# Kernel tuning notes

Measured on AMD Instinct MI355X. Metric: run time of the kernel, lower is better.

The kernel has to match this reference:

```python
import jax, jax.numpy as jnp
import numpy as np
from jax import lax

BIN_NUM = 48
CPG = BIN_NUM * 3            # 144 hidden channels
NOUT = BIN_NUM + 1           # 49 symbols
K = 5                        # masked conv kernel size
H, W = 256, 512
TABLE_TOTAL = 65536.0        # EntropyTable total frequency
SCALE = 2.0 / (BIN_NUM - 1.0)


def _causal_mask(include_center: bool) -> jnp.ndarray:
    # Raster-scan causal 5x5 mask: all rows above center, left of center in
    # center row; center tap only for 'hidden' (mask-B) layers.
    m = np.zeros((K, K), np.float32)
    c = K // 2
    m[:c, :] = 1.0
    m[c, :c] = 1.0
    if include_center:
        m[c, c] = 1.0
    return jnp.asarray(m)[None, None]  # broadcast over (O, I, kh, kw)


def _mconv(x, w, b, mask):
    # x: (N, C, H, W); w: (O, I, K, K)
    y = lax.conv_general_dilated(
        x, w * mask, window_strides=(1, 1), padding='SAME',
        dimension_numbers=('NCHW', 'OIHW', 'NCHW'))
    return y + b[None, :, None, None]


def setup_inputs() -> dict:
    key = jax.random.key(0)
    ks = jax.random.split(key, 8)
    # quantized code indices in [0, BIN_NUM)
    data = jax.random.randint(ks[0], (1, 1, H, W), 0, BIN_NUM).astype(jnp.float32)
    s0 = 1.0 / np.sqrt(1 * K * K)
    sr = 1.0 / np.sqrt(CPG * K * K)
    w0 = jax.random.normal(ks[1], (CPG, 1, K, K), jnp.float32) * s0
    b0 = jnp.zeros((CPG,), jnp.float32)
    # 5 residual blocks x 2 convs = 10 hidden masked convs, stacked
    wres = jax.random.normal(ks[2], (10, CPG, CPG, K, K), jnp.float32) * sr
    bres = jnp.zeros((10, CPG), jnp.float32)
    wl = jax.random.normal(ks[3], (NOUT, CPG, K, K), jnp.float32) * sr
    bl = jnp.zeros((NOUT,), jnp.float32)
    return {"data": data, "w0": w0, "b0": b0, "wres": wres, "bres": bres,
            "wl": wl, "bl": bl}


def reference(data, w0, b0, wres, bres, wl, bl):
    mask_a = _causal_mask(False)   # first layer excludes center pixel
    mask_b = _causal_mask(True)    # hidden layers include center pixel

    # Scale(-1, 2/(bin_num-1)): map codes [0, bin_num-1] -> [-1, 1]
    x = data * SCALE - 1.0
    x = jax.nn.relu(_mconv(x, w0, b0, mask_a))
    # 5 residual blocks: y = relu(conv(relu(conv(x)))) + x
    for i in range(5):
        h1 = jax.nn.relu(_mconv(x, wres[2 * i], bres[2 * i], mask_b))
        h2 = jax.nn.relu(_mconv(h1, wres[2 * i + 1], bres[2 * i + 1], mask_b))
        x = x + h2
    logits = _mconv(x, wl, bl, mask_b)          # (1, 49, H, W)

    # EntropyTable: per-pixel softmax -> cumulative frequency table (total 65536)
    probs = jax.nn.softmax(logits, axis=1)
    cdf = jnp.cumsum(probs, axis=1) * TABLE_TOTAL
    zeros = jnp.zeros((cdf.shape[0], 1) + cdf.shape[2:], cdf.dtype)
    vec = jnp.concatenate([zeros, cdf], axis=1)  # (1, 50, H, W)
    return vec
```

## Files before the change

### kernel.cpp

```cpp
#include <hip/hip_runtime.h>

#define HH 256
#define WW 512
#define CPG 144
#define NKG 18
#define WP 516
#define HPADR 258
#define XB_E ((size_t)NKG * HPADR * WP * 8)
#define NCH 59
#define KREAL 1872
#define SCALE_F (2.0f / 47.0f)

typedef __attribute__((ext_vector_type(8))) short short8;
typedef __attribute__((ext_vector_type(4))) float floatx4;

__device__ __forceinline__ unsigned short f2bf(float f) {
    unsigned u = __builtin_bit_cast(unsigned, f);
    u += 0x7FFFu + ((u >> 16) & 1u);
    return (unsigned short)(u >> 16);
}
__device__ __forceinline__ float bf2f(unsigned short h) {
    unsigned u = ((unsigned)h) << 16;
    return __builtin_bit_cast(float, u);
}
__device__ __forceinline__ void async16(const void* g, void* l) {
    __builtin_amdgcn_global_load_lds(
        (const __attribute__((address_space(1))) unsigned int*)g,
        (__attribute__((address_space(3))) unsigned int*)l, 16, 0, 0);
}
__device__ __forceinline__ void tap_decode(int t, int& kh, int& kw) {
    kh = t < 5 ? 0 : (t < 10 ? 1 : 2);
    kw = t - (t < 5 ? 0 : (t < 10 ? 5 : 10));
}
__device__ __forceinline__ unsigned aoff(int c, int lg) {
    int g = c * 4 + lg;
    if (g > 233) g = 233;
    int t = (g * 57) >> 10;
    int kgp = g - t * 18;
    int kh, kw; tap_decode(t, kh, kw);
    return (unsigned)(((kgp * 4 + kh) * 132 + kw) * 16);
}

__global__ void k_zero(float* __restrict__ p, size_t n4) {
    size_t i = (size_t)blockIdx.x * blockDim.x + threadIdx.x;
    size_t stride = (size_t)gridDim.x * blockDim.x;
    float4 z = make_float4(0.f, 0.f, 0.f, 0.f);
    for (; i < n4; i += stride) ((float4*)p)[i] = z;
}

__global__ void k_pack_hidden(const float* __restrict__ wres, unsigned short* __restrict__ wpk) {
    const int total = 10 * NCH * CPG * 32;
    int i = blockIdx.x * blockDim.x + threadIdx.x;
    int stride = gridDim.x * blockDim.x;
    for (; i < total; i += stride) {
        int kk = i & 31;
        int q  = i >> 5;
        int co = q % CPG;
        int c  = (q / CPG) % NCH;
        int l  = q / (CPG * NCH);
        int K = c * 32 + kk;
        float v = 0.f;
        if (K < KREAL) {
            int t = K / CPG, ci = K - t * CPG;
            int kh, kw; tap_decode(t, kh, kw);
            v = wres[(((size_t)(l * CPG + co) * CPG + ci) * 5 + kh) * 5 + kw];
        }
        wpk[i] = f2bf(v);
    }
}
__global__ void k_pack_final(const float* __restrict__ wl, unsigned short* __restrict__ wpkF) {
    const int total = NCH * 64 * 32;
    int i = blockIdx.x * blockDim.x + threadIdx.x;
    if (i >= total) return;
    int kk = i & 31;
    int co = (i >> 5) & 63;
    int c  = i >> 11;
    int K = c * 32 + kk;
    float v = 0.f;
    if (K < KREAL && co < 49) {
        int t = K / CPG, ci = K - t * CPG;
        int kh, kw; tap_decode(t, kh, kw);
        v = wl[(((size_t)co * CPG + ci) * 5 + kh) * 5 + kw];
    }
    wpkF[i] = f2bf(v);
}
__global__ void k_pack_small(const float* __restrict__ w0, const float* __restrict__ bl,
                             float* __restrict__ w0p, float* __restrict__ blp) {
    int i = blockIdx.x * blockDim.x + threadIdx.x;
    if (i < 12 * CPG) {
        int co = i % CPG, t = i / CPG;
        int kh, kw; tap_decode(t, kh, kw);
        w0p[i] = w0[co * 25 + kh * 5 + kw];
    } else if (i < 12 * CPG + 64) {
        int k = i - 12 * CPG;
        blp[k] = k < 49 ? bl[k] : 0.f;
    }
}

__global__ __launch_bounds__(384) void k_layer0(
    const float* __restrict__ data, const float* __restrict__ w0p,
    const float* __restrict__ b0, unsigned short* __restrict__ Xb) {
    const int lane = threadIdx.x;
    const int x = blockIdx.x * 64 + lane;
    const int y = blockIdx.y;

    float xv[12];
#pragma unroll
    for (int t = 0; t < 12; t++) {
        int kh, kw; tap_decode(t, kh, kw);
        int yy = y + kh - 2, xx = x + kw - 2;
        xv[t] = (yy >= 0 && xx >= 0 && xx < WW) ? data[yy * WW + xx] * SCALE_F - 1.0f : 0.f;
    }
#pragma unroll
    for (int kgi = 0; kgi < 3; kgi++) {
        int kg = threadIdx.y * 3 + kgi;
        float a8[8];
#pragma unroll
        for (int j = 0; j < 8; j++) a8[j] = 0.f;
#pragma unroll
        for (int t = 0; t < 12; t++)
#pragma unroll
            for (int j = 0; j < 8; j++)
                a8[j] = fmaf(w0p[t * CPG + kg * 8 + j], xv[t], a8[j]);
        short8 o;
#pragma unroll
        for (int j = 0; j < 8; j++)
            o[j] = (short)f2bf(fmaxf(a8[j] + b0[kg * 8 + j], 0.f));
        *(short8*)&Xb[((size_t)(kg * HPADR + y + 2) * WP + (x + 2)) * 8] = o;
    }
}

template<bool RES>
__global__ __launch_bounds__(768, 3) void k_conv(
    const unsigned short* __restrict__ in,
    const unsigned short* __restrict__ wq,
    const float* __restrict__ bias,
    const unsigned short* __restrict__ res,
    unsigned short* __restrict__ out) {
    __shared__ __align__(16) unsigned short As[NKG][4][132][8];
    const int tid  = threadIdx.x;
    const int lane = tid & 63;
    const int wid  = tid >> 6;
    const int ng   = wid % 3;
    const int r    = (wid / 3) & 1;
    const int ph   = wid / 6;
    const int lr = lane & 15;
    const int lg = lane >> 4;

    const int fid = blockIdx.x + (int)gridDim.x * blockIdx.y;
    const int swz = (fid & 7) * 64 + (fid >> 3);
    const int x0 = (swz & 3) * 128;
    const int y0 = (swz >> 2) * 2;

    floatx4 acc[4][3];
#pragma unroll
    for (int m = 0; m < 4; m++)
#pragma unroll
        for (int n = 0; n < 3; n++) acc[m][n] = (floatx4)0.f;

    for (int i = wid; i < 144; i += 12) {
        int half = i & 1;
        int rr   = (i >> 1) & 3;
        int kg   = i >> 3;
        async16(in + ((size_t)(kg * HPADR + y0 + rr) * WP + x0 + half * 64 + lane) * 8,
                &As[kg][rr][half * 64][0]);
    }
    if (tid < 288) {
        int kg = tid >> 4;
        int rr = (tid >> 2) & 3;
        int pxl = 128 + (tid & 3);
        *(short8*)&As[kg][rr][pxl][0] =
            *(const short8*)(in + ((size_t)(kg * HPADR + y0 + rr) * WP + x0 + pxl) * 8);
    }
    asm volatile("s_waitcnt vmcnt(0) lgkmcnt(0)" ::: "memory");
    __builtin_amdgcn_s_barrier();
    __builtin_amdgcn_sched_barrier(0);

    const char* abase = (const char*)&As[0][r][ph * 64 + lr][0];
    auto LDA = [&](int c, short8 (&a)[4]) {
        const char* ap = abase + aoff(c, lg);
#pragma unroll
        for (int m = 0; m < 4; ++m) a[m] = *(const short8*)(ap + m * 256);
    };
    auto LDB = [&](int c, short8 (&b)[3]) {
        const unsigned short* bp = wq + (size_t)c * 4608 + (ng * 48 + lr) * 32 + lg * 8;
#pragma unroll
        for (int n = 0; n < 3; ++n) b[n] = *(const short8*)(bp + n * 512);
    };
    auto CMP = [&](const short8 (&a)[4], const short8 (&b)[3]) {
        __builtin_amdgcn_sched_barrier(0);
        __builtin_amdgcn_s_setprio(1);
#pragma unroll
        for (int m = 0; m < 4; ++m)
#pragma unroll
            for (int n = 0; n < 3; ++n)
                acc[m][n] = __builtin_amdgcn_mfma_f32_16x16x32_bf16(a[m], b[n], acc[m][n], 0, 0, 0);
        __builtin_amdgcn_s_setprio(0);
        __builtin_amdgcn_sched_barrier(0);
    };

    short8 A0[4], A1[4], B0[3], B1[3], B2[3], B3[3];
    LDB(0, B0); LDB(1, B1); LDA(0, A0);
#pragma unroll 1
    for (int c = 0; c < 56; c += 4) {
        LDB(c + 2, B2); LDB(c + 3, B3);
        LDA(c + 1, A1); CMP(A0, B0);
        LDA(c + 2, A0); CMP(A1, B1);
        LDB(c + 4, B0); LDB(c + 5, B1);
        LDA(c + 3, A1); CMP(A0, B2);
        LDA(c + 4, A0); CMP(A1, B3);
    }
    LDB(58, B2);
    LDA(57, A1); CMP(A0, B0);
    LDA(58, A0); CMP(A1, B1);
    CMP(A0, B2);

#pragma unroll
    for (int n = 0; n < 3; ++n) {
        int co = ng * 48 + n * 16 + lr;
        float bv = bias[co];
        const size_t pb = ((size_t)((co >> 3) * HPADR + y0 + 2 + r) * WP + (x0 + 2)) * 8 + (co & 7);
#pragma unroll
        for (int m = 0; m < 4; ++m)
#pragma unroll
            for (int rr = 0; rr < 4; ++rr) {
                int px = ph * 64 + m * 16 + lg * 4 + rr;
                size_t o = pb + (size_t)px * 8;
                float v = fmaxf(acc[m][n][rr] + bv, 0.f);
                if (RES) v += bf2f(res[o]);
                out[o] = f2bf(v);
            }
    }
}

__global__ __launch_bounds__(512, 2) void k_logits(
    const unsigned short* __restrict__ in,
    const unsigned short* __restrict__ wq,
    const float* __restrict__ blp,
    float* __restrict__ logits) {
    __shared__ __align__(16) unsigned short As[NKG][4][132][8];
    const int tid  = threadIdx.x;
    const int lane = tid & 63;
    const int wid  = tid >> 6;
    const int ng   = wid & 1;
    const int r    = (wid >> 1) & 1;
    const int ph   = wid >> 2;
    const int lr = lane & 15;
    const int lg = lane >> 4;

    const int fid = blockIdx.x + (int)gridDim.x * blockIdx.y;
    const int swz = (fid & 7) * 64 + (fid >> 3);
    const int x0 = (swz & 3) * 128;
    const int y0 = (swz >> 2) * 2;

    floatx4 acc[4][2];
#pragma unroll
    for (int m = 0; m < 4; m++)
#pragma unroll
        for (int n = 0; n < 2; n++) acc[m][n] = (floatx4)0.f;

    for (int i = wid; i < 144; i += 8) {
        int half = i & 1;
        int rr   = (i >> 1) & 3;
        int kg   = i >> 3;
        async16(in + ((size_t)(kg * HPADR + y0 + rr) * WP + x0 + half * 64 + lane) * 8,
                &As[kg][rr][half * 64][0]);
    }
    if (tid < 288) {
        int kg = tid >> 4;
        int rr = (tid >> 2) & 3;
        int pxl = 128 + (tid & 3);
        *(short8*)&As[kg][rr][pxl][0] =
            *(const short8*)(in + ((size_t)(kg * HPADR + y0 + rr) * WP + x0 + pxl) * 8);
    }
    asm volatile("s_waitcnt vmcnt(0) lgkmcnt(0)" ::: "memory");
    __builtin_amdgcn_s_barrier();
    __builtin_amdgcn_sched_barrier(0);

    const char* abase = (const char*)&As[0][r][ph * 64 + lr][0];
    auto LDA = [&](int c, short8 (&a)[4]) {
        const char* ap = abase + aoff(c, lg);
#pragma unroll
        for (int m = 0; m < 4; ++m) a[m] = *(const short8*)(ap + m * 256);
    };
    auto LDB = [&](int c, short8 (&b)[2]) {
        const unsigned short* bp = wq + (size_t)c * 2048 + (ng * 32 + lr) * 32 + lg * 8;
#pragma unroll
        for (int n = 0; n < 2; ++n) b[n] = *(const short8*)(bp + n * 512);
    };
    auto CMP = [&](const short8 (&a)[4], const short8 (&b)[2]) {
        __builtin_amdgcn_sched_barrier(0);
        __builtin_amdgcn_s_setprio(1);
#pragma unroll
        for (int m = 0; m < 4; ++m)
#pragma unroll
            for (int n = 0; n < 2; ++n)
                acc[m][n] = __builtin_amdgcn_mfma_f32_16x16x32_bf16(a[m], b[n], acc[m][n], 0, 0, 0);
        __builtin_amdgcn_s_setprio(0);
        __builtin_amdgcn_sched_barrier(0);
    };

    short8 A0[4], A1[4], B0[2], B1[2], B2[2], B3[2];
    LDB(0, B0); LDB(1, B1); LDA(0, A0);
#pragma unroll 1
    for (int c = 0; c < 56; c += 4) {
        LDB(c + 2, B2); LDB(c + 3, B3);
        LDA(c + 1, A1); CMP(A0, B0);
        LDA(c + 2, A0); CMP(A1, B1);
        LDB(c + 4, B0); LDB(c + 5, B1);
        LDA(c + 3, A1); CMP(A0, B2);
        LDA(c + 4, A0); CMP(A1, B3);
    }
    LDB(58, B2);
    LDA(57, A1); CMP(A0, B0);
    LDA(58, A0); CMP(A1, B1);
    CMP(A0, B2);

#pragma unroll
    for (int n = 0; n < 2; ++n) {
        int co = ng * 32 + n * 16 + lr;
        float bv = blp[co];
#pragma unroll
        for (int m = 0; m < 4; ++m)
#pragma unroll
            for (int rr = 0; rr < 4; ++rr) {
                int px = ph * 64 + m * 16 + lg * 4 + rr;
                logits[((size_t)(y0 + r) * WW + x0 + px) * 64 + co] = acc[m][n][rr] + bv;
            }
    }
}

__global__ __launch_bounds__(256) void k_softmax(
    const float* __restrict__ lg, float* __restrict__ out) {
    const int px = blockIdx.x * 256 + threadIdx.x;
    const int y = blockIdx.y;
    const size_t p = (size_t)y * WW + px;
    const float* l = lg + p * 64;
    float v[49];
    float m = -1e30f;
#pragma unroll
    for (int k = 0; k < 49; k++) { v[k] = l[k]; m = fmaxf(m, v[k]); }
    float s = 0.f;
#pragma unroll
    for (int k = 0; k < 49; k++) {
        v[k] = exp2f((v[k] - m) * 1.44269504088896f);
        s += v[k];
    }
    const float inv = 65536.0f / s;
    out[p] = 0.f;
    float run = 0.f;
#pragma unroll
    for (int k = 0; k < 49; k++) {
        run += v[k];
        out[(size_t)(k + 1) * (HH * WW) + p] = run * inv;
    }
}

extern "C" void kernel_launch(void* const* d_in, const int* in_sizes, int n_in,
                              void* d_out, int out_size, void* d_ws, size_t ws_size,
                              hipStream_t stream) {
    (void)in_sizes; (void)n_in; (void)out_size; (void)ws_size;
    const float* data = (const float*)d_in[0];
    const float* w0   = (const float*)d_in[1];
    const float* b0   = (const float*)d_in[2];
    const float* wres = (const float*)d_in[3];
    const float* bres = (const float*)d_in[4];
    const float* wl   = (const float*)d_in[5];
    const float* bl   = (const float*)d_in[6];
    float* out = (float*)d_out;

    char* ws = (char*)d_ws;
    unsigned short* Xb   = (unsigned short*)ws;
    unsigned short* Hb   = Xb + XB_E;
    unsigned short* wpk  = Hb + XB_E;
    unsigned short* wpkF = wpk + (size_t)10 * NCH * CPG * 32;
    float* blp  = (float*)(wpkF + (size_t)NCH * 64 * 32);
    float* w0p  = blp + 64;
    float* logits = w0p + 1728;

    k_zero<<<2048, 256, 0, stream>>>((float*)ws, (2 * XB_E * 2) / 16);

    k_pack_hidden<<<2048, 256, 0, stream>>>(wres, wpk);
    k_pack_final<<<(NCH * 64 * 32 + 255) / 256, 256, 0, stream>>>(wl, wpkF);
    k_pack_small<<<7, 256, 0, stream>>>(w0, bl, w0p, blp);

    k_layer0<<<dim3(8, 256), dim3(64, 6), 0, stream>>>(data, w0p, b0, Xb);

    const size_t LSTRIDE = (size_t)NCH * CPG * 32;
    for (int i = 0; i < 5; i++) {
        k_conv<false><<<dim3(4, 128), 768, 0, stream>>>(
            Xb, wpk + (size_t)(2 * i) * LSTRIDE, bres + (2 * i) * CPG, Xb, Hb);
        k_conv<true><<<dim3(4, 128), 768, 0, stream>>>(
            Hb, wpk + (size_t)(2 * i + 1) * LSTRIDE, bres + (2 * i + 1) * CPG, Xb, Xb);
    }

    k_logits<<<dim3(4, 128), 512, 0, stream>>>(Xb, wpkF, blp, logits);
    k_softmax<<<dim3(2, 256), 256, 0, stream>>>(logits, out);
}
```

Before: 913.5 us.

## Retile convs to 4x64 pixel blocks and stage weights in LDS with triple buffering

```diff
diff --git a/kernel.cpp b/kernel.cpp
--- a/kernel.cpp
+++ b/kernel.cpp
@@ -32,13 +32,13 @@
     kh = t < 5 ? 0 : (t < 10 ? 1 : 2);
     kw = t - (t < 5 ? 0 : (t < 10 ? 5 : 10));
 }
-__device__ __forceinline__ unsigned aoff(int c, int lg) {
+__device__ __forceinline__ unsigned aoff6(int c, int lg) {
     int g = c * 4 + lg;
     if (g > 233) g = 233;
     int t = (g * 57) >> 10;
     int kgp = g - t * 18;
     int kh, kw; tap_decode(t, kh, kw);
-    return (unsigned)(((kgp * 4 + kh) * 132 + kw) * 16);
+    return (unsigned)(((kgp * 6 + kh) * 68 + kw) * 16);
 }
 
 __global__ void k_zero(float* __restrict__ p, size_t n4) {
@@ -49,16 +49,17 @@
 }
 
 __global__ void k_pack_hidden(const float* __restrict__ wres, unsigned short* __restrict__ wpk) {
-    const int total = 10 * NCH * CPG * 32;
+    const int total = 10 * NCH * 4 * CPG * 8;
     int i = blockIdx.x * blockDim.x + threadIdx.x;
     int stride = gridDim.x * blockDim.x;
     for (; i < total; i += stride) {
-        int kk = i & 31;
-        int q  = i >> 5;
-        int co = q % CPG;
-        int c  = (q / CPG) % NCH;
-        int l  = q / (CPG * NCH);
-        int K = c * 32 + kk;
+        int j  = i & 7;
+        int q  = i >> 3;
+        int co = q % CPG;  q /= CPG;
+        int lg = q & 3;    q >>= 2;
+        int c  = q % NCH;
+        int l  = q / NCH;
+        int K = c * 32 + lg * 8 + j;
         float v = 0.f;
         if (K < KREAL) {
             int t = K / CPG, ci = K - t * CPG;
@@ -69,13 +70,14 @@
     }
 }
 __global__ void k_pack_final(const float* __restrict__ wl, unsigned short* __restrict__ wpkF) {
-    const int total = NCH * 64 * 32;
+    const int total = NCH * 4 * 64 * 8;
     int i = blockIdx.x * blockDim.x + threadIdx.x;
     if (i >= total) return;
-    int kk = i & 31;
-    int co = (i >> 5) & 63;
+    int j  = i & 7;
+    int co = (i >> 3) & 63;
+    int lg = (i >> 9) & 3;
     int c  = i >> 11;
-    int K = c * 32 + kk;
+    int K = c * 32 + lg * 8 + j;
     float v = 0.f;
     if (K < KREAL && co < 49) {
         int t = K / CPG, ci = K - t * CPG;
@@ -137,20 +139,20 @@
     const float* __restrict__ bias,
     const unsigned short* __restrict__ res,
     unsigned short* __restrict__ out) {
-    __shared__ __align__(16) unsigned short As[NKG][4][132][8];
+    __shared__ __align__(16) unsigned short As[NKG][6][68][8];
+    __shared__ __align__(16) unsigned short Bs[3][4608];
     const int tid  = threadIdx.x;
     const int lane = tid & 63;
     const int wid  = tid >> 6;
     const int ng   = wid % 3;
-    const int r    = (wid / 3) & 1;
-    const int ph   = wid / 6;
+    const int r    = wid / 3;
     const int lr = lane & 15;
     const int lg = lane >> 4;
 
     const int fid = blockIdx.x + (int)gridDim.x * blockIdx.y;
     const int swz = (fid & 7) * 64 + (fid >> 3);
-    const int x0 = (swz & 3) * 128;
-    const int y0 = (swz >> 2) * 2;
+    const int x0 = (swz & 7) * 64;
+    const int y0 = (swz >> 3) * 4;
 
     floatx4 acc[4][3];
 #pragma unroll
@@ -158,37 +160,41 @@
 #pragma unroll
         for (int n = 0; n < 3; n++) acc[m][n] = (floatx4)0.f;
 
-    for (int i = wid; i < 144; i += 12) {
-        int half = i & 1;
-        int rr   = (i >> 1) & 3;
-        int kg   = i >> 3;
-        async16(in + ((size_t)(kg * HPADR + y0 + rr) * WP + x0 + half * 64 + lane) * 8,
-                &As[kg][rr][half * 64][0]);
-    }
-    if (tid < 288) {
-        int kg = tid >> 4;
-        int rr = (tid >> 2) & 3;
-        int pxl = 128 + (tid & 3);
-        *(short8*)&As[kg][rr][pxl][0] =
-            *(const short8*)(in + ((size_t)(kg * HPADR + y0 + rr) * WP + x0 + pxl) * 8);
+    for (int i = wid; i < 108; i += 12) {
+        int kg = i / 6, rr = i - (i / 6) * 6;
+        async16(in + ((size_t)(kg * HPADR + y0 + rr) * WP + x0 + lane) * 8,
+                &As[kg][rr][0][0]);
+    }
+    if (tid < 432) {
+        int kg = tid / 24;
+        int rem = tid - kg * 24;
+        int rr = rem >> 2;
+        int p  = rem & 3;
+        *(short8*)&As[kg][rr][64 + p][0] =
+            *(const short8*)(in + ((size_t)(kg * HPADR + y0 + rr) * WP + x0 + 64 + p) * 8);
+    }
+    for (int i = wid; i < 18; i += 12) {
+        int c = i / 9, s = i - (i / 9) * 9;
+        async16(wq + (size_t)c * 4608 + s * 512 + lane * 8, &Bs[c][s * 512]);
     }
     asm volatile("s_waitcnt vmcnt(0) lgkmcnt(0)" ::: "memory");
     __builtin_amdgcn_s_barrier();
     __builtin_amdgcn_sched_barrier(0);
 
-    const char* abase = (const char*)&As[0][r][ph * 64 + lr][0];
-    auto LDA = [&](int c, short8 (&a)[4]) {
-        const char* ap = abase + aoff(c, lg);
+    const char* abase = (const char*)As + ((r * 68) + lr) * 16;
+    int bufR = 0, bufW = 2;
+#pragma unroll 1
+    for (int c = 0; c < NCH; ++c) {
+        if (wid < 9 && c + 2 < NCH)
+            async16(wq + (size_t)(c + 2) * 4608 + wid * 512 + lane * 8,
+                    &Bs[bufW][wid * 512]);
+        short8 a[4], b[3];
+        const char* ap = abase + aoff6(c, lg);
 #pragma unroll
         for (int m = 0; m < 4; ++m) a[m] = *(const short8*)(ap + m * 256);
-    };
-    auto LDB = [&](int c, short8 (&b)[3]) {
-        const unsigned short* bp = wq + (size_t)c * 4608 + (ng * 48 + lr) * 32 + lg * 8;
-#pragma unroll
-        for (int n = 0; n < 3; ++n) b[n] = *(const short8*)(bp + n * 512);
-    };
-    auto CMP = [&](const short8 (&a)[4], const short8 (&b)[3]) {
-        __builtin_amdgcn_sched_barrier(0);
+        const unsigned short* bb = &Bs[bufR][lg * 1152 + (ng * 48 + lr) * 8];
+#pragma unroll
+        for (int n = 0; n < 3; ++n) b[n] = *(const short8*)(bb + n * 128);
         __builtin_amdgcn_s_setprio(1);
 #pragma unroll
         for (int m = 0; m < 4; ++m)
@@ -197,23 +203,12 @@
                 acc[m][n] = __builtin_amdgcn_mfma_f32_16x16x32_bf16(a[m], b[n], acc[m][n], 0, 0, 0);
         __builtin_amdgcn_s_setprio(0);
         __builtin_amdgcn_sched_barrier(0);
-    };
-
-    short8 A0[4], A1[4], B0[3], B1[3], B2[3], B3[3];
-    LDB(0, B0); LDB(1, B1); LDA(0, A0);
-#pragma unroll 1
-    for (int c = 0; c < 56; c += 4) {
-        LDB(c + 2, B2); LDB(c + 3, B3);
-        LDA(c + 1, A1); CMP(A0, B0);
-        LDA(c + 2, A0); CMP(A1, B1);
-        LDB(c + 4, B0); LDB(c + 5, B1);
-        LDA(c + 3, A1); CMP(A0, B2);
-        LDA(c + 4, A0); CMP(A1, B3);
-    }
-    LDB(58, B2);
-    LDA(57, A1); CMP(A0, B0);
-    LDA(58, A0); CMP(A1, B1);
-    CMP(A0, B2);
+        asm volatile("s_waitcnt vmcnt(1)" ::: "memory");
+        __builtin_amdgcn_s_barrier();
+        __builtin_amdgcn_sched_barrier(0);
+        bufR = bufR == 2 ? 0 : bufR + 1;
+        bufW = bufW == 2 ? 0 : bufW + 1;
+    }
 
 #pragma unroll
     for (int n = 0; n < 3; ++n) {
@@ -224,7 +219,7 @@
         for (int m = 0; m < 4; ++m)
 #pragma unroll
             for (int rr = 0; rr < 4; ++rr) {
-                int px = ph * 64 + m * 16 + lg * 4 + rr;
+                int px = m * 16 + lg * 4 + rr;
                 size_t o = pb + (size_t)px * 8;
                 float v = fmaxf(acc[m][n][rr] + bv, 0.f);
                 if (RES) v += bf2f(res[o]);
@@ -238,20 +233,20 @@
     const unsigned short* __restrict__ wq,
     const float* __restrict__ blp,
     float* __restrict__ logits) {
-    __shared__ __align__(16) unsigned short As[NKG][4][132][8];
+    __shared__ __align__(16) unsigned short As[NKG][6][68][8];
+    __shared__ __align__(16) unsigned short Bs[3][2048];
     const int tid  = threadIdx.x;
     const int lane = tid & 63;
     const int wid  = tid >> 6;
     const int ng   = wid & 1;
-    const int r    = (wid >> 1) & 1;
-    const int ph   = wid >> 2;
+    const int r    = wid >> 1;
     const int lr = lane & 15;
     const int lg = lane >> 4;
 
     const int fid = blockIdx.x + (int)gridDim.x * blockIdx.y;
     const int swz = (fid & 7) * 64 + (fid >> 3);
-    const int x0 = (swz & 3) * 128;
-    const int y0 = (swz >> 2) * 2;
+    const int x0 = (swz & 7) * 64;
+    const int y0 = (swz >> 3) * 4;
 
     floatx4 acc[4][2];
 #pragma unroll
@@ -259,37 +254,41 @@
 #pragma unroll
         for (int n = 0; n < 2; n++) acc[m][n] = (floatx4)0.f;
 
-    for (int i = wid; i < 144; i += 8) {
-        int half = i & 1;
-        int rr   = (i >> 1) & 3;
-        int kg   = i >> 3;
-        async16(in + ((size_t)(kg * HPADR + y0 + rr) * WP + x0 + half * 64 + lane) * 8,
-                &As[kg][rr][half * 64][0]);
-    }
-    if (tid < 288) {
-        int kg = tid >> 4;
-        int rr = (tid >> 2) & 3;
-        int pxl = 128 + (tid & 3);
-        *(short8*)&As[kg][rr][pxl][0] =
-            *(const short8*)(in + ((size_t)(kg * HPADR + y0 + rr) * WP + x0 + pxl) * 8);
+    for (int i = wid; i < 108; i += 8) {
+        int kg = i / 6, rr = i - (i / 6) * 6;
+        async16(in + ((size_t)(kg * HPADR + y0 + rr) * WP + x0 + lane) * 8,
+                &As[kg][rr][0][0]);
+    }
+    if (tid < 432) {
+        int kg = tid / 24;
+        int rem = tid - kg * 24;
+        int rr = rem >> 2;
+        int p  = rem & 3;
+        *(short8*)&As[kg][rr][64 + p][0] =
+            *(const short8*)(in + ((size_t)(kg * HPADR + y0 + rr) * WP + x0 + 64 + p) * 8);
+    }
+    for (int i = wid; i < 8; i += 8) {
+        int c = i >> 2, s = i & 3;
+        async16(wq + (size_t)c * 2048 + s * 512 + lane * 8, &Bs[c][s * 512]);
     }
     asm volatile("s_waitcnt vmcnt(0) lgkmcnt(0)" ::: "memory");
     __builtin_amdgcn_s_barrier();
     __builtin_amdgcn_sched_barrier(0);
 
-    const char* abase = (const char*)&As[0][r][ph * 64 + lr][0];
-    auto LDA = [&](int c, short8 (&a)[4]) {
-        const char* ap = abase + aoff(c, lg);
+    const char* abase = (const char*)As + ((r * 68) + lr) * 16;
+    int bufR = 0, bufW = 2;
+#pragma unroll 1
+    for (int c = 0; c < NCH; ++c) {
+        if (wid < 4 && c + 2 < NCH)
+            async16(wq + (size_t)(c + 2) * 2048 + wid * 512 + lane * 8,
+                    &Bs[bufW][wid * 512]);
+        short8 a[4], b[2];
+        const char* ap = abase + aoff6(c, lg);
 #pragma unroll
         for (int m = 0; m < 4; ++m) a[m] = *(const short8*)(ap + m * 256);
-    };
-    auto LDB = [&](int c, short8 (&b)[2]) {
-        const unsigned short* bp = wq + (size_t)c * 2048 + (ng * 32 + lr) * 32 + lg * 8;
-#pragma unroll
-        for (int n = 0; n < 2; ++n) b[n] = *(const short8*)(bp + n * 512);
-    };
-    auto CMP = [&](const short8 (&a)[4], const short8 (&b)[2]) {
-        __builtin_amdgcn_sched_barrier(0);
+        const unsigned short* bb = &Bs[bufR][lg * 512 + (ng * 32 + lr) * 8];
+#pragma unroll
+        for (int n = 0; n < 2; ++n) b[n] = *(const short8*)(bb + n * 128);
         __builtin_amdgcn_s_setprio(1);
 #pragma unroll
         for (int m = 0; m < 4; ++m)
@@ -298,23 +297,12 @@
                 acc[m][n] = __builtin_amdgcn_mfma_f32_16x16x32_bf16(a[m], b[n], acc[m][n], 0, 0, 0);
         __builtin_amdgcn_s_setprio(0);
         __builtin_amdgcn_sched_barrier(0);
-    };
-
-    short8 A0[4], A1[4], B0[2], B1[2], B2[2], B3[2];
-    LDB(0, B0); LDB(1, B1); LDA(0, A0);
-#pragma unroll 1
-    for (int c = 0; c < 56; c += 4) {
-        LDB(c + 2, B2); LDB(c + 3, B3);
-        LDA(c + 1, A1); CMP(A0, B0);
-        LDA(c + 2, A0); CMP(A1, B1);
-        LDB(c + 4, B0); LDB(c + 5, B1);
-        LDA(c + 3, A1); CMP(A0, B2);
-        LDA(c + 4, A0); CMP(A1, B3);
-    }
-    LDB(58, B2);
-    LDA(57, A1); CMP(A0, B0);
-    LDA(58, A0); CMP(A1, B1);
-    CMP(A0, B2);
+        asm volatile("s_waitcnt vmcnt(1)" ::: "memory");
+        __builtin_amdgcn_s_barrier();
+        __builtin_amdgcn_sched_barrier(0);
+        bufR = bufR == 2 ? 0 : bufR + 1;
+        bufW = bufW == 2 ? 0 : bufW + 1;
+    }
 
 #pragma unroll
     for (int n = 0; n < 2; ++n) {
@@ -324,7 +312,7 @@
         for (int m = 0; m < 4; ++m)
 #pragma unroll
             for (int rr = 0; rr < 4; ++rr) {
-                int px = ph * 64 + m * 16 + lg * 4 + rr;
+                int px = m * 16 + lg * 4 + rr;
                 logits[((size_t)(y0 + r) * WW + x0 + px) * 64 + co] = acc[m][n][rr] + bv;
             }
     }
@@ -373,27 +361,27 @@
     unsigned short* Xb   = (unsigned short*)ws;
     unsigned short* Hb   = Xb + XB_E;
     unsigned short* wpk  = Hb + XB_E;
-    unsigned short* wpkF = wpk + (size_t)10 * NCH * CPG * 32;
-    float* blp  = (float*)(wpkF + (size_t)NCH * 64 * 32);
+    unsigned short* wpkF = wpk + (size_t)10 * NCH * 4 * CPG * 8;
+    float* blp  = (float*)(wpkF + (size_t)NCH * 4 * 64 * 8);
     float* w0p  = blp + 64;
     float* logits = w0p + 1728;
 
     k_zero<<<2048, 256, 0, stream>>>((float*)ws, (2 * XB_E * 2) / 16);
 
     k_pack_hidden<<<2048, 256, 0, stream>>>(wres, wpk);
-    k_pack_final<<<(NCH * 64 * 32 + 255) / 256, 256, 0, stream>>>(wl, wpkF);
+    k_pack_final<<<(NCH * 4 * 64 * 8 + 255) / 256, 256, 0, stream>>>(wl, wpkF);
     k_pack_small<<<7, 256, 0, stream>>>(w0, bl, w0p, blp);
 
     k_layer0<<<dim3(8, 256), dim3(64, 6), 0, stream>>>(data, w0p, b0, Xb);
 
-    const size_t LSTRIDE = (size_t)NCH * CPG * 32;
+    const size_t LSTRIDE = (size_t)NCH * 4 * CPG * 8;
     for (int i = 0; i < 5; i++) {
-        k_conv<false><<<dim3(4, 128), 768, 0, stream>>>(
+        k_conv<false><<<dim3(8, 64), 768, 0, stream>>>(
             Xb, wpk + (size_t)(2 * i) * LSTRIDE, bres + (2 * i) * CPG, Xb, Hb);
-        k_conv<true><<<dim3(4, 128), 768, 0, stream>>>(
+        k_conv<true><<<dim3(8, 64), 768, 0, stream>>>(
             Hb, wpk + (size_t)(2 * i + 1) * LSTRIDE, bres + (2 * i + 1) * CPG, Xb, Xb);
     }
 
-    k_logits<<<dim3(4, 128), 512, 0, stream>>>(Xb, wpkF, blp, logits);
+    k_logits<<<dim3(8, 64), 512, 0, stream>>>(Xb, wpkF, blp, logits);
     k_softmax<<<dim3(2, 256), 256, 0, stream>>>(logits, out);
 }
```

After: 1.132 ms. 1.24x slower.

## Shrink conv tiles to 64 px with 4 padded output groups, 512-thread blocks

Applied to the files above, without the earlier changes.

```diff
diff --git a/kernel.cpp b/kernel.cpp
--- a/kernel.cpp
+++ b/kernel.cpp
@@ -3,6 +3,7 @@
 #define HH 256
 #define WW 512
 #define CPG 144
+#define NCO 192
 #define NKG 18
 #define WP 516
 #define HPADR 258
@@ -32,7 +33,15 @@
     kh = t < 5 ? 0 : (t < 10 ? 1 : 2);
     kw = t - (t < 5 ? 0 : (t < 10 ? 5 : 10));
 }
-__device__ __forceinline__ unsigned aoff(int c, int lg) {
+__device__ __forceinline__ unsigned aoff68(int c, int lg) {
+    int g = c * 4 + lg;
+    if (g > 233) g = 233;
+    int t = (g * 57) >> 10;
+    int kgp = g - t * 18;
+    int kh, kw; tap_decode(t, kh, kw);
+    return (unsigned)(((kgp * 4 + kh) * 68 + kw) * 16);
+}
+__device__ __forceinline__ unsigned aoff132(int c, int lg) {
     int g = c * 4 + lg;
     if (g > 233) g = 233;
     int t = (g * 57) >> 10;
@@ -49,18 +58,18 @@
 }
 
 __global__ void k_pack_hidden(const float* __restrict__ wres, unsigned short* __restrict__ wpk) {
-    const int total = 10 * NCH * CPG * 32;
+    const int total = 10 * NCH * NCO * 32;
     int i = blockIdx.x * blockDim.x + threadIdx.x;
     int stride = gridDim.x * blockDim.x;
     for (; i < total; i += stride) {
         int kk = i & 31;
         int q  = i >> 5;
-        int co = q % CPG;
-        int c  = (q / CPG) % NCH;
-        int l  = q / (CPG * NCH);
+        int co = q % NCO;  q /= NCO;
+        int c  = q % NCH;
+        int l  = q / NCH;
         int K = c * 32 + kk;
         float v = 0.f;
-        if (K < KREAL) {
+        if (K < KREAL && co < CPG) {
             int t = K / CPG, ci = K - t * CPG;
             int kh, kw; tap_decode(t, kh, kw);
             v = wres[(((size_t)(l * CPG + co) * CPG + ci) * 5 + kh) * 5 + kw];
@@ -131,26 +140,25 @@
 }
 
 template<bool RES>
-__global__ __launch_bounds__(768, 3) void k_conv(
+__global__ __launch_bounds__(512, 4) void k_conv(
     const unsigned short* __restrict__ in,
     const unsigned short* __restrict__ wq,
     const float* __restrict__ bias,
     const unsigned short* __restrict__ res,
     unsigned short* __restrict__ out) {
-    __shared__ __align__(16) unsigned short As[NKG][4][132][8];
+    __shared__ __align__(16) unsigned short As[NKG][4][68][8];
     const int tid  = threadIdx.x;
     const int lane = tid & 63;
     const int wid  = tid >> 6;
-    const int ng   = wid % 3;
-    const int r    = (wid / 3) & 1;
-    const int ph   = wid / 6;
+    const int ng   = wid & 3;
+    const int r    = wid >> 2;
     const int lr = lane & 15;
     const int lg = lane >> 4;
 
     const int fid = blockIdx.x + (int)gridDim.x * blockIdx.y;
-    const int swz = (fid & 7) * 64 + (fid >> 3);
-    const int x0 = (swz & 3) * 128;
-    const int y0 = (swz >> 2) * 2;
+    const int swz = (fid & 7) * 128 + (fid >> 3);
+    const int x0 = (swz & 7) * 64;
+    const int y0 = (swz >> 3) * 2;
 
     floatx4 acc[4][3];
 #pragma unroll
@@ -158,32 +166,31 @@
 #pragma unroll
         for (int n = 0; n < 3; n++) acc[m][n] = (floatx4)0.f;
 
-    for (int i = wid; i < 144; i += 12) {
-        int half = i & 1;
-        int rr   = (i >> 1) & 3;
-        int kg   = i >> 3;
-        async16(in + ((size_t)(kg * HPADR + y0 + rr) * WP + x0 + half * 64 + lane) * 8,
-                &As[kg][rr][half * 64][0]);
+    for (int i = wid; i < 72; i += 8) {
+        int rr = i & 3;
+        int kg = i >> 2;
+        async16(in + ((size_t)(kg * HPADR + y0 + rr) * WP + x0 + lane) * 8,
+                &As[kg][rr][0][0]);
     }
     if (tid < 288) {
         int kg = tid >> 4;
         int rr = (tid >> 2) & 3;
-        int pxl = 128 + (tid & 3);
-        *(short8*)&As[kg][rr][pxl][0] =
-            *(const short8*)(in + ((size_t)(kg * HPADR + y0 + rr) * WP + x0 + pxl) * 8);
+        int p  = tid & 3;
+        *(short8*)&As[kg][rr][64 + p][0] =
+            *(const short8*)(in + ((size_t)(kg * HPADR + y0 + rr) * WP + x0 + 64 + p) * 8);
     }
     asm volatile("s_waitcnt vmcnt(0) lgkmcnt(0)" ::: "memory");
     __builtin_amdgcn_s_barrier();
     __builtin_amdgcn_sched_barrier(0);
 
-    const char* abase = (const char*)&As[0][r][ph * 64 + lr][0];
+    const char* abase = (const char*)As + ((size_t)(r * 68) + lr) * 16;
     auto LDA = [&](int c, short8 (&a)[4]) {
-        const char* ap = abase + aoff(c, lg);
+        const char* ap = abase + aoff68(c, lg);
 #pragma unroll
         for (int m = 0; m < 4; ++m) a[m] = *(const short8*)(ap + m * 256);
     };
     auto LDB = [&](int c, short8 (&b)[3]) {
-        const unsigned short* bp = wq + (size_t)c * 4608 + (ng * 48 + lr) * 32 + lg * 8;
+        const unsigned short* bp = wq + (size_t)c * (NCO * 32) + (ng * 48 + lr) * 32 + lg * 8;
 #pragma unroll
         for (int n = 0; n < 3; ++n) b[n] = *(const short8*)(bp + n * 512);
     };
@@ -199,37 +206,38 @@
         __builtin_amdgcn_sched_barrier(0);
     };
 
-    short8 A0[4], A1[4], B0[3], B1[3], B2[3], B3[3];
-    LDB(0, B0); LDB(1, B1); LDA(0, A0);
+    short8 A0[4], A1[4], B0[3], B1[3];
+    LDB(0, B0); LDA(0, A0);
 #pragma unroll 1
-    for (int c = 0; c < 56; c += 4) {
-        LDB(c + 2, B2); LDB(c + 3, B3);
-        LDA(c + 1, A1); CMP(A0, B0);
-        LDA(c + 2, A0); CMP(A1, B1);
-        LDB(c + 4, B0); LDB(c + 5, B1);
-        LDA(c + 3, A1); CMP(A0, B2);
-        LDA(c + 4, A0); CMP(A1, B3);
-    }
-    LDB(58, B2);
-    LDA(57, A1); CMP(A0, B0);
-    LDA(58, A0); CMP(A1, B1);
-    CMP(A0, B2);
-
-#pragma unroll
-    for (int n = 0; n < 3; ++n) {
-        int co = ng * 48 + n * 16 + lr;
-        float bv = bias[co];
-        const size_t pb = ((size_t)((co >> 3) * HPADR + y0 + 2 + r) * WP + (x0 + 2)) * 8 + (co & 7);
-#pragma unroll
-        for (int m = 0; m < 4; ++m)
-#pragma unroll
-            for (int rr = 0; rr < 4; ++rr) {
-                int px = ph * 64 + m * 16 + lg * 4 + rr;
-                size_t o = pb + (size_t)px * 8;
-                float v = fmaxf(acc[m][n][rr] + bv, 0.f);
-                if (RES) v += bf2f(res[o]);
-                out[o] = f2bf(v);
-            }
+    for (int c = 0; c < 56; c += 2) {
+        LDB(c + 1, B1); LDA(c + 1, A1);
+        CMP(A0, B0);
+        LDB(c + 2, B0); LDA(c + 2, A0);
+        CMP(A1, B1);
+    }
+    LDB(57, B1); LDA(57, A1);
+    CMP(A0, B0);
+    LDB(58, B0); LDA(58, A0);
+    CMP(A1, B1);
+    CMP(A0, B0);
+
+    if (ng < 3) {
+#pragma unroll
+        for (int n = 0; n < 3; ++n) {
+            int co = ng * 48 + n * 16 + lr;
+            float bv = bias[co];
+            const size_t pb = ((size_t)((co >> 3) * HPADR + y0 + 2 + r) * WP + (x0 + 2)) * 8 + (co & 7);
+#pragma unroll
+            for (int m = 0; m < 4; ++m)
+#pragma unroll
+                for (int rr = 0; rr < 4; ++rr) {
+                    int px = m * 16 + lg * 4 + rr;
+                    size_t o = pb + (size_t)px * 8;
+                    float v = fmaxf(acc[m][n][rr] + bv, 0.f);
+                    if (RES) v += bf2f(res[o]);
+                    out[o] = f2bf(v);
+                }
+        }
     }
 }
 
@@ -277,9 +285,9 @@
     __builtin_amdgcn_s_barrier();
     __builtin_amdgcn_sched_barrier(0);
 
-    const char* abase = (const char*)&As[0][r][ph * 64 + lr][0];
+    const char* abase = (const char*)As + ((size_t)(r * 132) + ph * 64 + lr) * 16;
     auto LDA = [&](int c, short8 (&a)[4]) {
-        const char* ap = abase + aoff(c, lg);
+        const char* ap = abase + aoff132(c, lg);
 #pragma unroll
         for (int m = 0; m < 4; ++m) a[m] = *(const short8*)(ap + m * 256);
     };
@@ -373,7 +381,7 @@
     unsigned short* Xb   = (unsigned short*)ws;
     unsigned short* Hb   = Xb + XB_E;
     unsigned short* wpk  = Hb + XB_E;
-    unsigned short* wpkF = wpk + (size_t)10 * NCH * CPG * 32;
+    unsigned short* wpkF = wpk + (size_t)10 * NCH * NCO * 32;
     float* blp  = (float*)(wpkF + (size_t)NCH * 64 * 32);
     float* w0p  = blp + 64;
     float* logits = w0p + 1728;
@@ -386,11 +394,11 @@
 
     k_layer0<<<dim3(8, 256), dim3(64, 6), 0, stream>>>(data, w0p, b0, Xb);
 
-    const size_t LSTRIDE = (size_t)NCH * CPG * 32;
+    const size_t LSTRIDE = (size_t)NCH * NCO * 32;
     for (int i = 0; i < 5; i++) {
-        k_conv<false><<<dim3(4, 128), 768, 0, stream>>>(
+        k_conv<false><<<dim3(8, 128), 512, 0, stream>>>(
             Xb, wpk + (size_t)(2 * i) * LSTRIDE, bres + (2 * i) * CPG, Xb, Hb);
-        k_conv<true><<<dim3(4, 128), 768, 0, stream>>>(
+        k_conv<true><<<dim3(8, 128), 512, 0, stream>>>(
             Hb, wpk + (size_t)(2 * i + 1) * LSTRIDE, bres + (2 * i + 1) * CPG, Xb, Xb);
     }
 
```

New measurement: 1.046 ms. +14.5%, slower.
